# Optimization experiments

Hardware: AMD Instinct MI355X
Metric: run time of the kernel (lower is better)

## Reference

```python
import jax, jax.numpy as jnp
import numpy as np

N, IN_F, OUT_F, R = 8192, 4096, 4096, 16
ALPHA = 32
SCALING = ALPHA / R  # 2.0


def setup_inputs() -> dict:
    key = jax.random.key(0)
    k1, k2, k3, k4, k5 = jax.random.split(key, 5)
    return {
        "x": jax.random.normal(k1, (N, IN_F), dtype=jnp.float32),
        "W": jax.random.normal(k2, (OUT_F, IN_F), dtype=jnp.float32) * 0.02,
        "b": jax.random.normal(k3, (OUT_F,), dtype=jnp.float32) * 0.02,
        "lora_A": jax.random.normal(k4, (R, IN_F), dtype=jnp.float32) * 0.02,
        "lora_B": jax.random.normal(k5, (OUT_F, R), dtype=jnp.float32) * 0.02,
    }


def reference(x, W, b, lora_A, lora_B):
    # Base linear: x [N, in_f] @ W.T [in_f, out_f] + b -> [N, out_f]
    result = jnp.einsum('ni,oi->no', x, W) + b
    # LoRA path: (B @ (A @ x.T)).T * scaling == (x @ A.T) @ B.T * scaling
    lora = jnp.einsum('nr,or->no', jnp.einsum('ni,ri->nr', x, lora_A), lora_B)
    return result + lora * SCALING
```

## Files before the change

### kernel.cpp

```cpp
#include <hip/hip_runtime.h>
#include <hip/hip_bf16.h>
#include <stdint.h>

#define N_ROWS 8192
#define IN_F   4096
#define OUT_F  4096
#define R_LORA 16
#define KP     4160

typedef __bf16 bf16_t;
typedef __attribute__((ext_vector_type(8))) __bf16 bf16x8;
typedef __attribute__((ext_vector_type(4))) __bf16 bf16x4;
typedef __attribute__((ext_vector_type(4))) float  f32x4;
typedef __attribute__((ext_vector_type(16))) float f32x16;

__device__ __forceinline__ void load16_lds(const bf16_t* g, bf16_t* l) {
    auto gp = (const __attribute__((address_space(1))) void*)g;
    auto lp = (__attribute__((address_space(3))) void*)(uint32_t)(uintptr_t)l;
    __builtin_amdgcn_global_load_lds(gp, lp, 16, 0, 0);
}

#define PREPA_BLOCKS 2048

__global__ __launch_bounds__(256) void prep_fused(const float* __restrict__ x,
                                                  const float* __restrict__ W,
                                                  const float* __restrict__ bias,
                                                  const float* __restrict__ lA,
                                                  const float* __restrict__ lB,
                                                  bf16_t* __restrict__ Aw,
                                                  bf16_t* __restrict__ Bw) {
    int b = blockIdx.x;
    int t = threadIdx.x;
    if (b < PREPA_BLOCKS) {
        int row0 = b * 4;
        for (int rr = 0; rr < 4; ++rr) {
            int row = row0 + rr;
            const float4* xr = (const float4*)(x + (size_t)row * IN_F);
            bf16_t* ar = Aw + (size_t)row * KP;
            for (int s = t; s < 512; s += 256) {
                float4 f0 = xr[2 * s];
                float4 f1 = xr[2 * s + 1];
                bf16x8 v;
                v[0] = (bf16_t)f0.x; v[1] = (bf16_t)f0.y;
                v[2] = (bf16_t)f0.z; v[3] = (bf16_t)f0.w;
                v[4] = (bf16_t)f1.x; v[5] = (bf16_t)f1.y;
                v[6] = (bf16_t)f1.z; v[7] = (bf16_t)f1.w;
                *(bf16x8*)(ar + s * 8) = v;
            }
            if (t < 64) ar[IN_F + t] = (t == 0) ? (bf16_t)1.0f : (bf16_t)0.0f;
        }
    } else {
        int o0 = (b - PREPA_BLOCKS) * 4;
        float bl[4][R_LORA];
        for (int oo = 0; oo < 4; ++oo)
            for (int r = 0; r < R_LORA; ++r)
                bl[oo][r] = 2.0f * lB[(o0 + oo) * R_LORA + r];

        for (int j = 0; j < IN_F / (256 * 4); ++j) {
            int i4 = (j * 256 + t) * 4;
            f32x4 acc[4];
            for (int oo = 0; oo < 4; ++oo) {
                float4 w = *(const float4*)(W + (size_t)(o0 + oo) * IN_F + i4);
                acc[oo] = (f32x4){w.x, w.y, w.z, w.w};
            }
            for (int r = 0; r < R_LORA; ++r) {
                float4 a = *(const float4*)(lA + (size_t)r * IN_F + i4);
                for (int oo = 0; oo < 4; ++oo) {
                    acc[oo][0] += bl[oo][r] * a.x;
                    acc[oo][1] += bl[oo][r] * a.y;
                    acc[oo][2] += bl[oo][r] * a.z;
                    acc[oo][3] += bl[oo][r] * a.w;
                }
            }
            for (int oo = 0; oo < 4; ++oo) {
                bf16x4 v;
                v[0] = (bf16_t)acc[oo][0]; v[1] = (bf16_t)acc[oo][1];
                v[2] = (bf16_t)acc[oo][2]; v[3] = (bf16_t)acc[oo][3];
                *(bf16x4*)(Bw + (size_t)(o0 + oo) * KP + i4) = v;
            }
        }
        {
            int oo = t >> 6;
            int c  = IN_F + (t & 63);
            float v = (c == IN_F) ? bias[o0 + oo] : 0.0f;
            Bw[(size_t)(o0 + oo) * KP + c] = (bf16_t)v;
        }
    }
}

#define BM 128
#define BN 128
#define BK 64

__global__ __launch_bounds__(256) void gemm_bt(const bf16_t* __restrict__ A,
                                               const bf16_t* __restrict__ B,
                                               float* __restrict__ C) {
    __shared__ bf16_t As[BM * BK];
    __shared__ bf16_t Bs[BN * BK];

    int bid = blockIdx.x;
    int bn  = bid & 31;
    int bm  = bid >> 5;
    int rowBase = bm * BM;
    int colBase = bn * BN;

    int t    = threadIdx.x;
    int lane = t & 63;
    int wave = t >> 6;
    int wr   = wave >> 1, wc = wave & 1;
    int l31  = lane & 31;
    int lhi  = lane >> 5;
    int l7   = lane & 7;

    f32x16 acc[2][2];
    for (int i = 0; i < 2; ++i)
        for (int j = 0; j < 2; ++j)
            for (int r = 0; r < 16; ++r) acc[i][j][r] = 0.f;

    const int kIters = KP / BK;

    for (int kt = 0; kt < kIters; ++kt) {
        int k0 = kt * BK;
        for (int i = 0; i < 4; ++i) {
            int slot = i * 256 + t;
            int r  = slot >> 3;
            int p  = slot & 7;
            int srcOff = ((p ^ (r & 7)) * 8);
            load16_lds(A + (size_t)(rowBase + r) * KP + k0 + srcOff, &As[slot * 8]);
            load16_lds(B + (size_t)(colBase + r) * KP + k0 + srcOff, &Bs[slot * 8]);
        }
        __syncthreads();

        for (int ks = 0; ks < 4; ++ks) {
            int chunk = (ks << 1) + lhi;
            int posOff = (chunk ^ l7) * 8;
            bf16x8 af[2], bfg[2];
            for (int ti = 0; ti < 2; ++ti) {
                int row = wr * 64 + ti * 32 + l31;
                af[ti] = *(const bf16x8*)&As[row * BK + posOff];
            }
            for (int tj = 0; tj < 2; ++tj) {
                int col = wc * 64 + tj * 32 + l31;
                bfg[tj] = *(const bf16x8*)&Bs[col * BK + posOff];
            }
            for (int ti = 0; ti < 2; ++ti)
                for (int tj = 0; tj < 2; ++tj)
                    acc[ti][tj] = __builtin_amdgcn_mfma_f32_32x32x16_bf16(
                        af[ti], bfg[tj], acc[ti][tj], 0, 0, 0);
        }
        __syncthreads();
    }

    for (int ti = 0; ti < 2; ++ti) {
        int rB = rowBase + wr * 64 + ti * 32 + 4 * lhi;
        for (int tj = 0; tj < 2; ++tj) {
            int col = colBase + wc * 64 + tj * 32 + l31;
            for (int reg = 0; reg < 16; ++reg) {
                int row = rB + (reg & 3) + 8 * (reg >> 2);
                C[(size_t)row * OUT_F + col] = acc[ti][tj][reg];
            }
        }
    }
}

extern "C" void kernel_launch(void* const* d_in, const int* in_sizes, int n_in,
                              void* d_out, int out_size, void* d_ws, size_t ws_size,
                              hipStream_t stream) {
    const float* x  = (const float*)d_in[0];
    const float* W  = (const float*)d_in[1];
    const float* b  = (const float*)d_in[2];
    const float* lA = (const float*)d_in[3];
    const float* lB = (const float*)d_in[4];
    float* out = (float*)d_out;

    bf16_t* Aw = (bf16_t*)d_ws;
    bf16_t* Bw = Aw + (size_t)N_ROWS * KP;

    prep_fused<<<PREPA_BLOCKS + OUT_F / 4, 256, 0, stream>>>(x, W, b, lA, lB, Aw, Bw);
    gemm_bt<<<(N_ROWS / BM) * (OUT_F / BN), 256, 0, stream>>>(Aw, Bw, out);
}
```

Baseline: 548.4 us.

## Rewrite GEMM as 256x256 tile, 8-wave, double-buffered LDS pipeline with interleaved loads

The GEMM now uses 256x256 output tiles on 512 threads and double-buffers LDS so that global-to-LDS loads for the next K step are issued in quarters between the four MFMA phases of the current step. It also adds a block-index swizzle for L2 locality, raises MFMA priority with setprio, and synchronises with explicit vmcnt waits plus barriers. The aim is to hide memory latency behind MFMA work and raise arithmetic intensity per tile. In exchange it needs 128KB of LDS and many accumulator registers, which limits occupancy, and it depends on the hand-counted vmcnt values being correct.

```diff
diff --git a/kernel.cpp b/kernel.cpp
--- a/kernel.cpp
+++ b/kernel.cpp
@@ -88,76 +88,141 @@
     }
 }
 
-#define BM 128
-#define BN 128
+#define BM 256
+#define BN 256
 #define BK 64
-
-__global__ __launch_bounds__(256) void gemm_bt(const bf16_t* __restrict__ A,
-                                               const bf16_t* __restrict__ B,
-                                               float* __restrict__ C) {
-    __shared__ bf16_t As[BM * BK];
-    __shared__ bf16_t Bs[BN * BK];
+#define NT (KP / BK)
+
+#define VMB(n) do { asm volatile("s_waitcnt vmcnt(" #n ")" ::: "memory"); \
+                    __builtin_amdgcn_s_barrier(); } while (0)
+
+template<int Q>
+__device__ __forceinline__ void phase_mma(const bf16_t* Ab, const bf16_t* Bb,
+                                          f32x16 (&acc)[4][2],
+                                          int rowA0, int colB0, int lhi, int l7) {
+    constexpr int qa = Q & 1, qb = Q >> 1;
+    bf16x8 a0[4], a1[4], bb[4];
+#pragma unroll
+    for (int ks = 0; ks < 4; ++ks) {
+        int pos = ((((ks << 1) | lhi)) ^ l7) << 3;
+        a0[ks] = *(const bf16x8*)&Ab[(qa * 128 + rowA0) * BK + pos];
+        a1[ks] = *(const bf16x8*)&Ab[(qa * 128 + rowA0 + 32) * BK + pos];
+        bb[ks] = *(const bf16x8*)&Bb[(qb * 128 + colB0) * BK + pos];
+    }
+    __builtin_amdgcn_s_setprio(1);
+#pragma unroll
+    for (int ks = 0; ks < 4; ++ks) {
+        acc[Q][0] = __builtin_amdgcn_mfma_f32_32x32x16_bf16(a0[ks], bb[ks], acc[Q][0], 0, 0, 0);
+        acc[Q][1] = __builtin_amdgcn_mfma_f32_32x32x16_bf16(a1[ks], bb[ks], acc[Q][1], 0, 0, 0);
+    }
+    __builtin_amdgcn_s_setprio(0);
+}
+
+__global__ __launch_bounds__(512, 2) void gemm_bt(const bf16_t* __restrict__ A,
+                                                  const bf16_t* __restrict__ B,
+                                                  float* __restrict__ C) {
+    __shared__ __align__(16) bf16_t lds[2][2][BM * BK];
 
     int bid = blockIdx.x;
-    int bn  = bid & 31;
-    int bm  = bid >> 5;
+    int swz = (bid & 7) * 64 + (bid >> 3);
+    int bm  = swz & 31;
+    int bn  = swz >> 5;
     int rowBase = bm * BM;
     int colBase = bn * BN;
 
-    int t    = threadIdx.x;
-    int lane = t & 63;
-    int wave = t >> 6;
-    int wr   = wave >> 1, wc = wave & 1;
-    int l31  = lane & 31;
-    int lhi  = lane >> 5;
-    int l7   = lane & 7;
-
-    f32x16 acc[2][2];
-    for (int i = 0; i < 2; ++i)
-        for (int j = 0; j < 2; ++j)
-            for (int r = 0; r < 16; ++r) acc[i][j][r] = 0.f;
-
-    const int kIters = KP / BK;
-
-    for (int kt = 0; kt < kIters; ++kt) {
-        int k0 = kt * BK;
-        for (int i = 0; i < 4; ++i) {
-            int slot = i * 256 + t;
-            int r  = slot >> 3;
-            int p  = slot & 7;
-            int srcOff = ((p ^ (r & 7)) * 8);
-            load16_lds(A + (size_t)(rowBase + r) * KP + k0 + srcOff, &As[slot * 8]);
-            load16_lds(B + (size_t)(colBase + r) * KP + k0 + srcOff, &Bs[slot * 8]);
-        }
-        __syncthreads();
-
-        for (int ks = 0; ks < 4; ++ks) {
-            int chunk = (ks << 1) + lhi;
-            int posOff = (chunk ^ l7) * 8;
-            bf16x8 af[2], bfg[2];
-            for (int ti = 0; ti < 2; ++ti) {
-                int row = wr * 64 + ti * 32 + l31;
-                af[ti] = *(const bf16x8*)&As[row * BK + posOff];
-            }
-            for (int tj = 0; tj < 2; ++tj) {
-                int col = wc * 64 + tj * 32 + l31;
-                bfg[tj] = *(const bf16x8*)&Bs[col * BK + posOff];
-            }
-            for (int ti = 0; ti < 2; ++ti)
-                for (int tj = 0; tj < 2; ++tj)
-                    acc[ti][tj] = __builtin_amdgcn_mfma_f32_32x32x16_bf16(
-                        af[ti], bfg[tj], acc[ti][tj], 0, 0, 0);
-        }
-        __syncthreads();
-    }
-
-    for (int ti = 0; ti < 2; ++ti) {
-        int rB = rowBase + wr * 64 + ti * 32 + 4 * lhi;
-        for (int tj = 0; tj < 2; ++tj) {
-            int col = colBase + wc * 64 + tj * 32 + l31;
+    const int t    = threadIdx.x;
+    const int lane = t & 63;
+    const int wave = t >> 6;
+    const int l31  = lane & 31;
+    const int lhi  = lane >> 5;
+    const int l7   = lane & 7;
+    const int wr   = wave >> 2;
+    const int wcp  = wave & 3;
+    const int rowA0 = wr * 64 + l31;
+    const int colB0 = wcp * 32 + l31;
+
+    uint32_t srcA[4], srcB[4];
+#pragma unroll
+    for (int s = 0; s < 4; ++s) {
+        int c = s * 512 + t;
+        int r = c >> 3, p = c & 7;
+        uint32_t off = (uint32_t)(r * KP + ((p ^ (r & 7)) << 3));
+        srcA[s] = (uint32_t)(rowBase * KP) + off;
+        srcB[s] = (uint32_t)(colBase * KP) + off;
+    }
+
+    auto stageA = [&](int half, int bsel, int k0) {
+#pragma unroll
+        for (int s2 = 0; s2 < 2; ++s2) {
+            int s = half * 2 + s2;
+            load16_lds(A + srcA[s] + k0, &lds[bsel][0][(s * 512 + t) * 8]);
+        }
+    };
+    auto stageB = [&](int half, int bsel, int k0) {
+#pragma unroll
+        for (int s2 = 0; s2 < 2; ++s2) {
+            int s = half * 2 + s2;
+            load16_lds(B + srcB[s] + k0, &lds[bsel][1][(s * 512 + t) * 8]);
+        }
+    };
+
+    f32x16 acc[4][2];
+#pragma unroll
+    for (int q = 0; q < 4; ++q)
+#pragma unroll
+        for (int i = 0; i < 2; ++i)
+#pragma unroll
+            for (int r = 0; r < 16; ++r) acc[q][i][r] = 0.f;
+
+    stageA(0, 0, 0);
+    stageB(0, 0, 0);
+    stageA(1, 0, 0);
+    stageB(1, 0, 0);
+
+    int kt = 0;
+    for (; kt < NT - 1; ++kt) {
+        const int bsel = kt & 1;
+        const int nb   = bsel ^ 1;
+        const int k1   = (kt + 1) * BK;
+        const bf16_t* Ab = &lds[bsel][0][0];
+        const bf16_t* Bb = &lds[bsel][1][0];
+
+        VMB(4);
+        stageA(0, nb, k1);
+        phase_mma<0>(Ab, Bb, acc, rowA0, colB0, lhi, l7);
+        VMB(4);
+        stageB(0, nb, k1);
+        phase_mma<1>(Ab, Bb, acc, rowA0, colB0, lhi, l7);
+        VMB(4);
+        stageA(1, nb, k1);
+        phase_mma<2>(Ab, Bb, acc, rowA0, colB0, lhi, l7);
+        stageB(1, nb, k1);
+        phase_mma<3>(Ab, Bb, acc, rowA0, colB0, lhi, l7);
+    }
+    {
+        const int bsel = kt & 1;
+        const bf16_t* Ab = &lds[bsel][0][0];
+        const bf16_t* Bb = &lds[bsel][1][0];
+        VMB(4);
+        phase_mma<0>(Ab, Bb, acc, rowA0, colB0, lhi, l7);
+        VMB(2);
+        phase_mma<1>(Ab, Bb, acc, rowA0, colB0, lhi, l7);
+        VMB(0);
+        phase_mma<2>(Ab, Bb, acc, rowA0, colB0, lhi, l7);
+        phase_mma<3>(Ab, Bb, acc, rowA0, colB0, lhi, l7);
+    }
+
+#pragma unroll
+    for (int q = 0; q < 4; ++q) {
+        const int qa = q & 1, qb = q >> 1;
+#pragma unroll
+        for (int i = 0; i < 2; ++i) {
+            int rB  = rowBase + qa * 128 + wr * 64 + i * 32 + 4 * lhi;
+            int col = colBase + qb * 128 + wcp * 32 + l31;
+#pragma unroll
             for (int reg = 0; reg < 16; ++reg) {
                 int row = rB + (reg & 3) + 8 * (reg >> 2);
-                C[(size_t)row * OUT_F + col] = acc[ti][tj][reg];
+                C[(size_t)row * OUT_F + col] = acc[q][i][reg];
             }
         }
     }
@@ -177,5 +242,5 @@
     bf16_t* Bw = Aw + (size_t)N_ROWS * KP;
 
     prep_fused<<<PREPA_BLOCKS + OUT_F / 4, 256, 0, stream>>>(x, W, b, lA, lB, Aw, Bw);
-    gemm_bt<<<(N_ROWS / BM) * (OUT_F / BN), 256, 0, stream>>>(Aw, Bw, out);
-}
+    gemm_bt<<<(N_ROWS / BM) * (OUT_F / BN), 512, 0, stream>>>(Aw, Bw, out);
+}
```

New measurement: 565.4 us. 3.1% more time.
